# Kernel tuning notes

Hardware: AMD Instinct MI355X
Metric: run time of the kernel (lower is better)

Reference implementation:

```python
import jax, jax.numpy as jnp
import numpy as np

B, N, NGT, C, H, W = 2, 64, 8, 17, 64, 64
HMS_W, SCORE_W, OFF_W = 2.0, 1.0, 1.0
ALPHA, GAMMA, BETA = 0.25, 2.0, 4.0


def setup_inputs() -> dict:
    key = jax.random.key(0)
    ks = jax.random.split(key, 7)
    pred_hms = jax.random.normal(ks[0], (B, N, C, H, W), jnp.float32)
    pred_scores = jax.random.normal(ks[1], (B, N, 1), jnp.float32)
    pred_offsets = jax.random.normal(ks[2], (B, N, C, 2), jnp.float32)
    # gt heatmaps in [0, 0.9), then force one exact 1.0 peak per (b, n, c)
    gt = jax.random.uniform(ks[3], (B, NGT, C, H * W), jnp.float32) * 0.9
    peak = jax.random.randint(ks[4], (B, NGT, C), 0, H * W)
    bi, ni, ci = jnp.meshgrid(jnp.arange(B), jnp.arange(NGT), jnp.arange(C), indexing='ij')
    gt = gt.at[bi, ni, ci, peak].set(1.0)
    keep = (jax.random.uniform(ks[5], (B, NGT, C)) > 0.2).astype(jnp.float32)
    gt_heatmaps = (gt * keep[..., None]).reshape(B, NGT, C, H, W)
    gt_offsets = jax.random.uniform(ks[6], (B, NGT, C, 2), jnp.float32)
    return {"pred_hms": pred_hms, "gt_heatmaps": gt_heatmaps,
            "pred_scores": pred_scores, "pred_offsets": pred_offsets,
            "gt_offsets": gt_offsets}


def _bce_logits(x, t):
    # numerically stable binary_cross_entropy_with_logits
    return jnp.maximum(x, 0.0) - x * t + jnp.log1p(jnp.exp(-jnp.abs(x)))


def _single_cost(ph, ps, gh, po, go):
    # ph: [N, C, HW], ps: [N, 1], gh: [n, C, HW], po: [N, C, 2], go: [n, C, 2]
    no_kp = gh.sum(-1) == 0                       # [n, C]
    valid = (~no_kp).astype(ph.dtype)             # [n, C]
    num_kp = jnp.maximum(valid.sum(-1), 1.0)      # [n]
    # ---- heatmap focal cost ----
    x = ph[:, None]                               # [N, 1, C, HW]
    p = jax.nn.sigmoid(x)
    ce = _bce_logits(x, gh[None]) * valid[None, :, :, None]  # [N, n, C, HW]
    eq1 = (gh == 1.0).astype(ph.dtype)
    neq1 = 1.0 - eq1
    p_t = ((1.0 - p) * eq1[None] + p * neq1[None]) ** GAMMA
    ratio = eq1 + ((1.0 - gh) * neq1) ** BETA
    hms_cost = (ce * p_t * ratio[None]).sum((-1, -2)) / num_kp[None]  # [N, n]
    # ---- score focal cost (targets always 1.0) ----
    sp = jax.nn.sigmoid(ps)                       # [N, 1]
    score = ALPHA * _bce_logits(ps, 1.0) * (1.0 - sp) ** GAMMA
    score_cost = jnp.broadcast_to(score, (ph.shape[0], gh.shape[0]))  # [N, n]
    # ---- offset L2 cost ----
    pos = jax.nn.sigmoid(po)[:, None]             # [N, 1, C, 2]
    oc = ((pos - go[None]) ** 2).sum(-1) * valid[None]  # [N, n, C]
    off_cost = oc.sum(-1) / num_kp[None] / 2.0    # [N, n]
    return hms_cost * HMS_W + score_cost * SCORE_W + off_cost * OFF_W


def reference(pred_hms, gt_heatmaps, pred_scores, pred_offsets, gt_offsets):
    ph = pred_hms.reshape(B, N, C, H * W)
    gh = gt_heatmaps.reshape(B, NGT, C, H * W)
    # per-image cost matrices [B, N, n] (Hungarian assignment is a CPU
    # post-process in the original and excluded from the GPU math)
    return jax.vmap(_single_cost)(ph, pred_scores, gh, pred_offsets, gt_offsets)
```

## Files before the change

kernel.cpp:

```cpp
#include <hip/hip_runtime.h>

#define BB 2
#define NN 64
#define GG 8
#define CC 17
#define HWW 4096

__global__ __launch_bounds__(256) void k_valid(const float* __restrict__ gh,
                                               float* __restrict__ validws) {
    int bid = blockIdx.x;
    int b = bid / (GG * CC);
    int g = (bid / CC) % GG;
    int c = bid % CC;
    const float* base = gh + (size_t)bid * HWW;
    int tid = threadIdx.x;
    float m = 0.f;
    for (int i = tid; i < HWW; i += 256) m = fmaxf(m, base[i]);
    #pragma unroll
    for (int off = 32; off; off >>= 1) m = fmaxf(m, __shfl_down(m, off, 64));
    __shared__ float red[4];
    int lane = tid & 63, wid = tid >> 6;
    if (lane == 0) red[wid] = m;
    __syncthreads();
    if (tid == 0) {
        float mm = fmaxf(fmaxf(red[0], red[1]), fmaxf(red[2], red[3]));
        validws[((b * CC + c) << 3) + g] = (mm > 0.f) ? 1.f : 0.f;
    }
}

__global__ __launch_bounds__(256) void k_hms(const float* __restrict__ ph,
                                             const float* __restrict__ gh,
                                             float* __restrict__ S1) {
    int bid = blockIdx.x;
    int c = bid % CC;
    int bn = bid / CC;
    int b = bn >> 6;
    int tid = threadIdx.x;
    const float* phb = ph + (size_t)bid * HWW;
    const float* gh0 = gh + ((size_t)(b * GG) * CC + c) * HWW;

    float acc[GG];
    #pragma unroll
    for (int g = 0; g < GG; ++g) acc[g] = 0.f;

    for (int i = tid; i < HWW; i += 256) {
        float x = phb[i];
        float ax = fabsf(x);
        float ex = __expf(-ax);
        float l1p = __logf(1.f + ex);
        float sp = fmaxf(x, 0.f) + l1p;
        float r = 1.f / (1.f + ex);
        float p = (x >= 0.f) ? r : (1.f - r);
        float p2 = p * p;
        float A  = sp * p2;
        float Bv = x * p2;
        float omp = 1.f - p;
        float post = (sp - x) * omp * omp;
        #pragma unroll
        for (int g = 0; g < GG; ++g) {
            float t = gh0[(size_t)g * (CC * HWW) + i];
            float om = 1.f - t;
            float om2 = om * om;
            float u = om2 * om2;
            float contrib = fmaf(A, u, -(Bv * (t * u)));
            acc[g] += (t == 1.f) ? post : contrib;
        }
    }

    __shared__ float red[4][GG];
    int lane = tid & 63, wid = tid >> 6;
    #pragma unroll
    for (int g = 0; g < GG; ++g) {
        float v = acc[g];
        #pragma unroll
        for (int off = 32; off; off >>= 1) v += __shfl_down(v, off, 64);
        if (lane == 0) red[wid][g] = v;
    }
    __syncthreads();
    if (tid < GG) {
        float s = red[0][tid] + red[1][tid] + red[2][tid] + red[3][tid];
        S1[((size_t)bid << 3) + tid] = s;
    }
}

__global__ __launch_bounds__(256) void k_final(const float* __restrict__ S1,
                                               const float* __restrict__ validws,
                                               const float* __restrict__ ps,
                                               const float* __restrict__ po,
                                               const float* __restrict__ go,
                                               float* __restrict__ out) {
    int idx = blockIdx.x * blockDim.x + threadIdx.x;
    if (idx >= BB * NN * GG) return;
    int g = idx & 7;
    int bn = idx >> 3;
    int b = bn >> 6;

    float nk = 0.f, hsum = 0.f, osum = 0.f;
    #pragma unroll
    for (int c = 0; c < CC; ++c) {
        float v = validws[((b * CC + c) << 3) + g];
        nk += v;
        hsum += v * S1[(((size_t)bn * CC + c) << 3) + g];
        int poi = (bn * CC + c) * 2;
        int goi = ((b * GG + g) * CC + c) * 2;
        float s0 = 1.f / (1.f + __expf(-po[poi]));
        float s1 = 1.f / (1.f + __expf(-po[poi + 1]));
        float d0 = s0 - go[goi];
        float d1 = s1 - go[goi + 1];
        osum += v * fmaf(d0, d0, d1 * d1);
    }
    float nkp = fmaxf(nk, 1.f);

    float s = ps[bn];
    float ax = fabsf(s);
    float ex = __expf(-ax);
    float spn = fmaxf(-s, 0.f) + __logf(1.f + ex);
    float r = 1.f / (1.f + ex);
    float sg = (s >= 0.f) ? r : (1.f - r);
    float om = 1.f - sg;
    float score = 0.25f * spn * om * om;

    out[idx] = 2.f * (hsum / nkp) + score + 0.5f * (osum / nkp);
}

extern "C" void kernel_launch(void* const* d_in, const int* in_sizes, int n_in,
                              void* d_out, int out_size, void* d_ws, size_t ws_size,
                              hipStream_t stream) {
    const float* ph = (const float*)d_in[0];
    const float* gh = (const float*)d_in[1];
    const float* ps = (const float*)d_in[2];
    const float* po = (const float*)d_in[3];
    const float* go = (const float*)d_in[4];
    float* out = (float*)d_out;

    float* S1 = (float*)d_ws;
    float* validws = S1 + (size_t)BB * NN * CC * GG;

    k_valid<<<BB * GG * CC, 256, 0, stream>>>(gh, validws);
    k_hms<<<BB * NN * CC, 256, 0, stream>>>(ph, gh, S1);
    k_final<<<(BB * NN * GG + 255) / 256, 256, 0, stream>>>(S1, validws, ps, po, go, out);
}
```

Baseline: 114.9 us.

## Tile k_hms over 4 predictions and split HW to reuse gt heatmap loads

Each k_hms block now handles 4 predictions for one (b,c) and half of the HW range. The per-pixel gt terms (u, t*u, eq1 mask) are computed once and reused across the 4 predictions, which cuts gt heatmap global reads about fourfold. The select on t==1 becomes branchless FMA chains. k_final sums the two HW-chunk partials, and the block count drops from 2176 to 1088 while each thread holds 32 accumulators, so register pressure rises.

```diff
diff --git a/kernel.cpp b/kernel.cpp
--- a/kernel.cpp
+++ b/kernel.cpp
@@ -5,6 +5,11 @@
 #define GG 8
 #define CC 17
 #define HWW 4096
+
+#define TN 4
+#define NTILES (NN / TN)
+#define HCH 2
+#define CHUNK (HWW / HCH)
 
 __global__ __launch_bounds__(256) void k_valid(const float* __restrict__ gh,
                                                float* __restrict__ validws) {
@@ -30,60 +35,85 @@
 
 __global__ __launch_bounds__(256) void k_hms(const float* __restrict__ ph,
                                              const float* __restrict__ gh,
-                                             float* __restrict__ S1) {
+                                             float* __restrict__ S2) {
     int bid = blockIdx.x;
-    int c = bid % CC;
-    int bn = bid / CC;
-    int b = bn >> 6;
+    int hc = bid & (HCH - 1);
+    int nt = (bid / HCH) % NTILES;
+    int bc = bid / (HCH * NTILES);
+    int b = bc / CC;
+    int c = bc % CC;
     int tid = threadIdx.x;
-    const float* phb = ph + (size_t)bid * HWW;
-    const float* gh0 = gh + ((size_t)(b * GG) * CC + c) * HWW;
 
-    float acc[GG];
+    const int strideC = CC * HWW;
+    const float* gh0 = gh + ((size_t)b * GG * CC + c) * HWW + hc * CHUNK;
+    const float* ph0 = ph + ((size_t)b * NN * CC + (size_t)nt * TN * CC + c) * HWW + hc * CHUNK;
+
+    float acc[TN][GG];
     #pragma unroll
-    for (int g = 0; g < GG; ++g) acc[g] = 0.f;
+    for (int j = 0; j < TN; ++j)
+        #pragma unroll
+        for (int g = 0; g < GG; ++g) acc[j][g] = 0.f;
 
-    for (int i = tid; i < HWW; i += 256) {
-        float x = phb[i];
-        float ax = fabsf(x);
-        float ex = __expf(-ax);
-        float l1p = __logf(1.f + ex);
-        float sp = fmaxf(x, 0.f) + l1p;
-        float r = 1.f / (1.f + ex);
-        float p = (x >= 0.f) ? r : (1.f - r);
-        float p2 = p * p;
-        float A  = sp * p2;
-        float Bv = x * p2;
-        float omp = 1.f - p;
-        float post = (sp - x) * omp * omp;
+    for (int i = tid; i < CHUNK; i += 256) {
+        float u[GG], tu[GG], e[GG];
         #pragma unroll
         for (int g = 0; g < GG; ++g) {
-            float t = gh0[(size_t)g * (CC * HWW) + i];
+            float t = gh0[(size_t)g * strideC + i];
             float om = 1.f - t;
             float om2 = om * om;
-            float u = om2 * om2;
-            float contrib = fmaf(A, u, -(Bv * (t * u)));
-            acc[g] += (t == 1.f) ? post : contrib;
+            float uu = om2 * om2;
+            u[g] = uu;
+            tu[g] = t * uu;
+            e[g] = (t == 1.f) ? 1.f : 0.f;
+        }
+        float xs[TN];
+        #pragma unroll
+        for (int j = 0; j < TN; ++j) xs[j] = ph0[(size_t)j * strideC + i];
+        #pragma unroll
+        for (int j = 0; j < TN; ++j) {
+            float x = xs[j];
+            float ax = fabsf(x);
+            float ex = __expf(-ax);
+            float l1p = __logf(1.f + ex);
+            float sp = fmaxf(x, 0.f) + l1p;
+            float r = 1.f / (1.f + ex);
+            float p = (x >= 0.f) ? r : (1.f - r);
+            float p2 = p * p;
+            float A   = sp * p2;
+            float nBv = -(x * p2);
+            float omp = 1.f - p;
+            float post = (sp - x) * omp * omp;
+            #pragma unroll
+            for (int g = 0; g < GG; ++g) {
+                float a = acc[j][g];
+                a = fmaf(A, u[g], a);
+                a = fmaf(nBv, tu[g], a);
+                a = fmaf(post, e[g], a);
+                acc[j][g] = a;
+            }
         }
     }
 
-    __shared__ float red[4][GG];
+    __shared__ float red[4][TN * GG];
     int lane = tid & 63, wid = tid >> 6;
     #pragma unroll
-    for (int g = 0; g < GG; ++g) {
-        float v = acc[g];
+    for (int j = 0; j < TN; ++j) {
         #pragma unroll
-        for (int off = 32; off; off >>= 1) v += __shfl_down(v, off, 64);
-        if (lane == 0) red[wid][g] = v;
+        for (int g = 0; g < GG; ++g) {
+            float v = acc[j][g];
+            #pragma unroll
+            for (int off = 32; off; off >>= 1) v += __shfl_down(v, off, 64);
+            if (lane == 0) red[wid][j * GG + g] = v;
+        }
     }
     __syncthreads();
-    if (tid < GG) {
+    if (tid < TN * GG) {
         float s = red[0][tid] + red[1][tid] + red[2][tid] + red[3][tid];
-        S1[((size_t)bid << 3) + tid] = s;
+        S2[(size_t)bid * (TN * GG) + tid] = s;
     }
 }
 
-__global__ __launch_bounds__(256) void k_final(const float* __restrict__ S1,
+__global__ __launch_bounds__(256) void k_final(const float* __restrict__ S2,
                                                const float* __restrict__ validws,
                                                const float* __restrict__ ps,
                                                const float* __restrict__ po,
@@ -94,13 +124,22 @@
     int g = idx & 7;
     int bn = idx >> 3;
     int b = bn >> 6;
+    int n = bn & 63;
+    int nt = n / TN;
+    int j = n % TN;
 
     float nk = 0.f, hsum = 0.f, osum = 0.f;
     #pragma unroll
     for (int c = 0; c < CC; ++c) {
         float v = validws[((b * CC + c) << 3) + g];
         nk += v;
-        hsum += v * S1[(((size_t)bn * CC + c) << 3) + g];
+        float s = 0.f;
+        #pragma unroll
+        for (int hc = 0; hc < HCH; ++hc) {
+            size_t bid2 = ((size_t)(b * CC + c) * NTILES + nt) * HCH + hc;
+            s += S2[bid2 * (TN * GG) + j * GG + g];
+        }
+        hsum += v * s;
         int poi = (bn * CC + c) * 2;
         int goi = ((b * GG + g) * CC + c) * 2;
         float s0 = 1.f / (1.f + __expf(-po[poi]));
@@ -133,10 +172,11 @@
     const float* go = (const float*)d_in[4];
     float* out = (float*)d_out;
 
-    float* S1 = (float*)d_ws;
-    float* validws = S1 + (size_t)BB * NN * CC * GG;
+    const int n_s2 = BB * CC * NTILES * HCH * TN * GG;
+    float* S2 = (float*)d_ws;
+    float* validws = S2 + n_s2;
 
     k_valid<<<BB * GG * CC, 256, 0, stream>>>(gh, validws);
-    k_hms<<<BB * NN * CC, 256, 0, stream>>>(ph, gh, S1);
-    k_final<<<(BB * NN * GG + 255) / 256, 256, 0, stream>>>(S1, validws, ps, po, go, out);
+    k_hms<<<BB * CC * NTILES * HCH, 256, 0, stream>>>(ph, gh, S2);
+    k_final<<<(BB * NN * GG + 255) / 256, 256, 0, stream>>>(S2, validws, ps, po, go, out);
 }
```

Result: no change. 114.6 us (-0.3%).
